# Performance work log

Hardware: AMD Instinct MI355X
Metric: run time of the kernel (lower is better)

Reference implementation:

```python
import jax, jax.numpy as jnp
import numpy as np

L, H, D, FF = 12, 12, 768, 3072          # ViT-B/16
PS, GRID = 16, 14
NP = GRID * GRID                          # 196 patches
NT = NP + 1                               # 197 tokens (cls + patches)
B = 64
NC = 100                                  # classes
POS_G = (0, 1)
POS_E = (2, 3, 4)
LEN_G, LEN_E = 5, 20
GL, EL = len(POS_G), len(POS_E)
E_POOL = 10                               # task_num


def _ln(x, g, b, eps=1e-6):
    m = x.mean(-1, keepdims=True)
    v = ((x - m) ** 2).mean(-1, keepdims=True)
    return (x - m) * jax.lax.rsqrt(v + eps) * g + b


def _mlp(x, w1, b1, w2, b2):
    return jax.nn.gelu(x @ w1.T + b1, approximate=False) @ w2.T + b2


def _attn(q, k, v):
    # q: [B,Nq,C], k/v: [B,Nk,C] (Nk may include prefix prompt tokens)
    Bq, Nq, C = q.shape
    hd = C // H
    q = q.reshape(Bq, Nq, H, hd).transpose(0, 2, 1, 3)
    k = k.reshape(Bq, -1, H, hd).transpose(0, 2, 1, 3)
    v = v.reshape(Bq, -1, H, hd).transpose(0, 2, 1, 3)
    a = jax.nn.softmax(jnp.einsum('bhqd,bhkd->bhqk', q, k) * (hd ** -0.5), axis=-1)
    o = jnp.einsum('bhqk,bhkd->bhqd', a, v)
    return o.transpose(0, 2, 1, 3).reshape(Bq, Nq, C)


def setup_inputs() -> dict:
    key = jax.random.key(0)
    ks = iter(jax.random.split(key, 24))
    s = 0.02
    return {
        'inputs':    jax.random.normal(next(ks), (B, 3, 224, 224), jnp.float32),
        'patch_w':   jax.random.normal(next(ks), (D, 3, PS, PS), jnp.float32) * s,
        'patch_b':   jnp.zeros((D,), jnp.float32),
        'cls_token': jax.random.normal(next(ks), (1, 1, D), jnp.float32) * s,
        'pos_embed': jax.random.normal(next(ks), (1, NT, D), jnp.float32) * s,
        'ln1_g':  jnp.ones((L, D), jnp.float32),
        'ln1_b':  jnp.zeros((L, D), jnp.float32),
        'qkv_w':  jax.random.normal(next(ks), (L, 3 * D, D), jnp.float32) * s,
        'qkv_b':  jnp.zeros((L, 3 * D), jnp.float32),
        'proj_w': jax.random.normal(next(ks), (L, D, D), jnp.float32) * s,
        'proj_b': jnp.zeros((L, D), jnp.float32),
        'ln2_g':  jnp.ones((L, D), jnp.float32),
        'ln2_b':  jnp.zeros((L, D), jnp.float32),
        'fc1_w':  jax.random.normal(next(ks), (L, FF, D), jnp.float32) * s,
        'fc1_b':  jnp.zeros((L, FF), jnp.float32),
        'fc2_w':  jax.random.normal(next(ks), (L, D, FF), jnp.float32) * s,
        'fc2_b':  jnp.zeros((L, D), jnp.float32),
        'norm_g': jnp.ones((D,), jnp.float32),
        'norm_b': jnp.zeros((D,), jnp.float32),
        'head_w': jax.random.normal(next(ks), (NC, D), jnp.float32) * s,
        'head_b': jnp.zeros((NC,), jnp.float32),
        'g_prompt': jax.random.normal(next(ks), (1, 2 * GL * LEN_G, D), jnp.float32) * s,
        'e_key':    jax.random.normal(next(ks), (E_POOL, D), jnp.float32),
        'e_prompt': jax.random.normal(next(ks), (E_POOL, 2 * EL * LEN_E, D), jnp.float32) * s,
    }


def _forward(inputs, patch_w, patch_b, cls_token, pos_embed, ln1_g, ln1_b,
             qkv_w, qkv_b, proj_w, proj_b, ln2_g, ln2_b, fc1_w, fc1_b,
             fc2_w, fc2_b, norm_g, norm_b, head_w, head_b,
             g_prompt, e_key, e_prompt):
    Bn = inputs.shape[0]
    # --- patch embed (conv k16 s16 == unfold + linear); under torch.no_grad ---
    x = inputs.reshape(Bn, 3, GRID, PS, GRID, PS).transpose(0, 2, 4, 1, 3, 5)
    x = x.reshape(Bn, NP, 3 * PS * PS) @ patch_w.reshape(D, -1).T + patch_b
    tok = jnp.concatenate([jnp.broadcast_to(cls_token, (Bn, 1, D)), x], axis=1)
    tok = jax.lax.stop_gradient(tok)  # token_appended computed in no_grad block
    # --- frozen query pass through plain ViT blocks ---
    q = tok + pos_embed
    for i in range(L):
        xn = _ln(q, ln1_g[i], ln1_b[i])
        qq, kk, vv = jnp.split(xn @ qkv_w[i].T + qkv_b[i], 3, axis=-1)
        q = q + _attn(qq, kk, vv) @ proj_w[i].T + proj_b[i]
        q = q + _mlp(_ln(q, ln2_g[i], ln2_b[i]), fc1_w[i], fc1_b[i], fc2_w[i], fc2_b[i])
    query = jax.lax.stop_gradient(_ln(q, norm_g, norm_b)[:, 0])  # [B, D]
    # --- prompt selection (eval path: cosine-sim top-1 from e-pool) ---
    qn = query / jnp.linalg.norm(query, axis=-1, keepdims=True)
    kn = e_key / jnp.linalg.norm(e_key, axis=-1, keepdims=True)
    idx = jnp.argmax(qn @ kn.T, axis=-1)                       # [B]
    cls_pe = pos_embed[0, 0]                                   # [D]
    g_p = jnp.broadcast_to(g_prompt[0].reshape(1, 2 * GL, LEN_G, D),
                           (Bn, 2 * GL, LEN_G, D)) + cls_pe
    e_p = e_prompt[idx].reshape(Bn, 2 * EL, LEN_E, D) + cls_pe
    # --- prefix-tuning pass: prompts concatenated to K/V only ---
    x = tok + pos_embed
    for n in range(L):
        xn = _ln(x, ln1_g[n], ln1_b[n])
        ks_, vs_ = [xn], [xn]
        if n in POS_G:
            j = POS_G.index(n)
            ks_.append(g_p[:, 2 * j]); vs_.append(g_p[:, 2 * j + 1])
        if n in POS_E:
            j = POS_E.index(n)
            ks_.append(e_p[:, 2 * j]); vs_.append(e_p[:, 2 * j + 1])
        xk = jnp.concatenate(ks_, axis=1) if len(ks_) > 1 else xn
        xv = jnp.concatenate(vs_, axis=1) if len(vs_) > 1 else xn
        qh = xn @ qkv_w[n][:D].T + qkv_b[n][:D]
        kh = xk @ qkv_w[n][D:2 * D].T + qkv_b[n][D:2 * D]
        vh = xv @ qkv_w[n][2 * D:].T + qkv_b[n][2 * D:]
        x = x + _attn(qh, kh, vh) @ proj_w[n].T + proj_b[n]
        x = x + _mlp(_ln(x, ln2_g[n], ln2_b[n]), fc1_w[n], fc1_b[n], fc2_w[n], fc2_b[n])
    x = _ln(x, norm_g, norm_b)
    return x[:, 0] @ head_w.T + head_b  # [B, NC]


def reference(inputs, patch_w, patch_b, cls_token, pos_embed, ln1_g, ln1_b,
              qkv_w, qkv_b, proj_w, proj_b, ln2_g, ln2_b, fc1_w, fc1_b,
              fc2_w, fc2_b, norm_g, norm_b, head_w, head_b,
              g_prompt, e_key, e_prompt):
    return _forward(inputs, patch_w, patch_b, cls_token, pos_embed, ln1_g, ln1_b,
                    qkv_w, qkv_b, proj_w, proj_b, ln2_g, ln2_b, fc1_w, fc1_b,
                    fc2_w, fc2_b, norm_g, norm_b, head_w, head_b,
                    g_prompt, e_key, e_prompt)
```

## Files before the change

kernel.cpp:

```cpp
#include <hip/hip_runtime.h>

typedef unsigned short ushort_t;
typedef __attribute__((ext_vector_type(8))) __bf16 bf16x8;
typedef __attribute__((ext_vector_type(4))) float f32x4;
typedef __attribute__((ext_vector_type(4))) unsigned int u32x4;
typedef __attribute__((ext_vector_type(4))) unsigned short u16x4;
typedef __attribute__((ext_vector_type(4))) float fl4;

#define AS1(p) ((const __attribute__((address_space(1))) void*)(p))
#define AS3(p) ((__attribute__((address_space(3))) void*)(p))

__device__ __forceinline__ ushort_t f2bf(float f) {
    unsigned u = __float_as_uint(f);
    u += 0x7FFFu + ((u >> 16) & 1u);
    return (ushort_t)(u >> 16);
}

__device__ __forceinline__ bf16x8 ld_bf8(const ushort_t* p) {
    return __builtin_bit_cast(bf16x8, *(const u32x4*)p);
}

__global__ void cvt_kernel(const float* __restrict__ in, ushort_t* __restrict__ out, int n4)
{
    int i = blockIdx.x * 256 + threadIdx.x;
    if (i >= n4) return;
    fl4 f = ((const fl4*)in)[i];
    u16x4 h;
    h.x = f2bf(f.x); h.y = f2bf(f.y); h.z = f2bf(f.z); h.w = f2bf(f.w);
    ((u16x4*)out)[i] = h;
}

template<int OBF, int ADD, int GELU>
__global__ __launch_bounds__(256)
void gemm_kernel(const ushort_t* __restrict__ A, const ushort_t* __restrict__ W,
                 const float* __restrict__ bias, void* __restrict__ Cv,
                 int M, int N, int K)
{
    __shared__ ushort_t As[128 * 32];
    __shared__ ushort_t Ws[128 * 32];
    const int tid  = threadIdx.x;
    const int lane = tid & 63, wv = tid >> 6;
    const int quad = lane >> 4, l16 = lane & 15;
    const int m0 = blockIdx.x * 128, n0 = blockIdx.y * 128;
    const int wm = (wv >> 1) * 64, wn = (wv & 1) * 64;

    f32x4 acc[4][4];
#pragma unroll
    for (int i = 0; i < 4; ++i)
#pragma unroll
        for (int j = 0; j < 4; ++j) acc[i][j] = (f32x4){0.f, 0.f, 0.f, 0.f};

    const int lr = lane >> 2, lc = (lane & 3) * 8;
    const ushort_t* gA0 = A + (size_t)(m0 + wv * 16 + lr) * K + lc;
    const ushort_t* gA1 = gA0 + (size_t)64 * K;
    const ushort_t* gW0 = W + (size_t)(n0 + wv * 16 + lr) * K + lc;
    const ushort_t* gW1 = gW0 + (size_t)64 * K;
    ushort_t* lA0 = As + wv * 512;
    ushort_t* lA1 = As + (wv + 4) * 512;
    ushort_t* lW0 = Ws + wv * 512;
    ushort_t* lW1 = Ws + (wv + 4) * 512;

    for (int kt = 0; kt < K; kt += 32) {
        __builtin_amdgcn_global_load_lds(AS1(gA0 + kt), AS3(lA0), 16, 0, 0);
        __builtin_amdgcn_global_load_lds(AS1(gA1 + kt), AS3(lA1), 16, 0, 0);
        __builtin_amdgcn_global_load_lds(AS1(gW0 + kt), AS3(lW0), 16, 0, 0);
        __builtin_amdgcn_global_load_lds(AS1(gW1 + kt), AS3(lW1), 16, 0, 0);
        __syncthreads();
        bf16x8 af[4], bfr[4];
#pragma unroll
        for (int i = 0; i < 4; ++i) af[i]  = ld_bf8(As + (wm + i * 16 + l16) * 32 + quad * 8);
#pragma unroll
        for (int j = 0; j < 4; ++j) bfr[j] = ld_bf8(Ws + (wn + j * 16 + l16) * 32 + quad * 8);
#pragma unroll
        for (int i = 0; i < 4; ++i)
#pragma unroll
            for (int j = 0; j < 4; ++j)
                acc[i][j] = __builtin_amdgcn_mfma_f32_16x16x32_bf16(af[i], bfr[j], acc[i][j], 0, 0, 0);
        __syncthreads();
    }

    float* Cf = (float*)Cv;
    ushort_t* Ch = (ushort_t*)Cv;
#pragma unroll
    for (int j = 0; j < 4; ++j) {
        int n = n0 + wn + j * 16 + l16;
        float bv = bias[n];
#pragma unroll
        for (int i = 0; i < 4; ++i) {
            int mb = m0 + wm + i * 16 + quad * 4;
#pragma unroll
            for (int r = 0; r < 4; ++r) {
                int m = mb + r;
                if (m < M) {
                    float v = acc[i][j][r] + bv;
                    if (GELU) v = 0.5f * v * (1.f + erff(v * 0.70710678118654752f));
                    size_t off = (size_t)m * N + n;
                    if (OBF) {
                        Ch[off] = f2bf(v);
                    } else {
                        float o = v;
                        if (ADD) o += Cf[off];
                        Cf[off] = o;
                    }
                }
            }
        }
    }
}

__global__ __launch_bounds__(256)
void attn_kernel(const ushort_t* __restrict__ qkv, const ushort_t* __restrict__ pk,
                 const ushort_t* __restrict__ pv, int plen, int pbs,
                 ushort_t* __restrict__ out)
{
    __shared__ ushort_t KV[224 * 72];
    __shared__ ushort_t Ps[64 * 232];
    const int tid  = threadIdx.x;
    const int lane = tid & 63, wv = tid >> 6;
    const int quad = lane >> 4, l16 = lane & 15;
    const int b = blockIdx.x / 12, h = blockIdx.x % 12;
    const int q0 = blockIdx.y * 64;
    const int Nk = 197 + plen;

    for (int i = tid; i < 224 * 8; i += 256) {
        int tok = i >> 3, c = (i & 7) * 8;
        u32x4 v = (u32x4){0, 0, 0, 0};
        if (tok < 197)
            v = *(const u32x4*)(qkv + (size_t)(b * 197 + tok) * 2304 + 768 + h * 64 + c);
        else if (tok < Nk)
            v = *(const u32x4*)(pk + (size_t)(b * pbs + (tok - 197)) * 768 + h * 64 + c);
        *(u32x4*)(KV + tok * 72 + c) = v;
    }
    __syncthreads();

    bf16x8 qf0 = __builtin_bit_cast(bf16x8, (u32x4){0, 0, 0, 0});
    bf16x8 qf1 = qf0;
    int qrow = q0 + wv * 16 + l16;
    if (qrow < 197) {
        const ushort_t* qp = qkv + (size_t)(b * 197 + qrow) * 2304 + h * 64 + quad * 8;
        qf0 = ld_bf8(qp);
        qf1 = ld_bf8(qp + 32);
    }

    f32x4 sarr[14];
#pragma unroll
    for (int t = 0; t < 14; ++t) {
        f32x4 s = (f32x4){0.f, 0.f, 0.f, 0.f};
        bf16x8 k0 = ld_bf8(KV + (t * 16 + l16) * 72 + quad * 8);
        bf16x8 k1 = ld_bf8(KV + (t * 16 + l16) * 72 + 32 + quad * 8);
        s = __builtin_amdgcn_mfma_f32_16x16x32_bf16(qf0, k0, s, 0, 0, 0);
        s = __builtin_amdgcn_mfma_f32_16x16x32_bf16(qf1, k1, s, 0, 0, 0);
        if (t * 16 + l16 >= Nk) s = (f32x4){-1e30f, -1e30f, -1e30f, -1e30f};
        sarr[t] = s;
    }

    float mx[4] = {-1e30f, -1e30f, -1e30f, -1e30f};
#pragma unroll
    for (int t = 0; t < 14; ++t)
#pragma unroll
        for (int r = 0; r < 4; ++r) mx[r] = fmaxf(mx[r], sarr[t][r]);
#pragma unroll
    for (int off = 8; off >= 1; off >>= 1)
#pragma unroll
        for (int r = 0; r < 4; ++r) mx[r] = fmaxf(mx[r], __shfl_xor(mx[r], off));

    float sm[4] = {0.f, 0.f, 0.f, 0.f};
#pragma unroll
    for (int t = 0; t < 14; ++t)
#pragma unroll
        for (int r = 0; r < 4; ++r) {
            float p = __expf((sarr[t][r] - mx[r]) * 0.125f);
            sm[r] += p;
            Ps[(wv * 16 + quad * 4 + r) * 232 + t * 16 + l16] = f2bf(p);
        }
#pragma unroll
    for (int off = 8; off >= 1; off >>= 1)
#pragma unroll
        for (int r = 0; r < 4; ++r) sm[r] += __shfl_xor(sm[r], off);
    float rs[4];
#pragma unroll
    for (int r = 0; r < 4; ++r) rs[r] = 1.f / sm[r];
    __syncthreads();

    for (int i = tid; i < 224 * 8; i += 256) {
        int tok = i >> 3, c = (i & 7) * 8;
        u32x4 v = (u32x4){0, 0, 0, 0};
        if (tok < 197)
            v = *(const u32x4*)(qkv + (size_t)(b * 197 + tok) * 2304 + 1536 + h * 64 + c);
        else if (tok < Nk)
            v = *(const u32x4*)(pv + (size_t)(b * pbs + (tok - 197)) * 768 + h * 64 + c);
        ushort_t tmp[8];
        *(u32x4*)tmp = v;
#pragma unroll
        for (int jj = 0; jj < 8; ++jj) KV[(c + jj) * 232 + tok] = tmp[jj];
    }
    __syncthreads();

    f32x4 oc[4];
#pragma unroll
    for (int j = 0; j < 4; ++j) oc[j] = (f32x4){0.f, 0.f, 0.f, 0.f};
#pragma unroll
    for (int ks = 0; ks < 7; ++ks) {
        bf16x8 pf = ld_bf8(Ps + (wv * 16 + l16) * 232 + ks * 32 + quad * 8);
#pragma unroll
        for (int j = 0; j < 4; ++j) {
            bf16x8 vf = ld_bf8(KV + (j * 16 + l16) * 232 + ks * 32 + quad * 8);
            oc[j] = __builtin_amdgcn_mfma_f32_16x16x32_bf16(pf, vf, oc[j], 0, 0, 0);
        }
    }
#pragma unroll
    for (int j = 0; j < 4; ++j) {
        int hd = h * 64 + j * 16 + l16;
#pragma unroll
        for (int r = 0; r < 4; ++r) {
            int qr = q0 + wv * 16 + quad * 4 + r;
            if (qr < 197) out[(size_t)(b * 197 + qr) * 768 + hd] = f2bf(oc[j][r] * rs[r]);
        }
    }
}

__global__ __launch_bounds__(256)
void ln_kernel(const float* __restrict__ x, const float* __restrict__ g,
               const float* __restrict__ bt, ushort_t* __restrict__ out)
{
    const int row = blockIdx.x, tid = threadIdx.x;
    const float* xr = x + (size_t)row * 768;
    float v0 = xr[tid], v1 = xr[tid + 256], v2 = xr[tid + 512];
    float s = v0 + v1 + v2;
    float s2 = v0 * v0 + v1 * v1 + v2 * v2;
#pragma unroll
    for (int off = 32; off >= 1; off >>= 1) {
        s  += __shfl_xor(s, off);
        s2 += __shfl_xor(s2, off);
    }
    __shared__ float red[8];
    if ((tid & 63) == 0) { red[tid >> 6] = s; red[(tid >> 6) + 4] = s2; }
    __syncthreads();
    float S  = red[0] + red[1] + red[2] + red[3];
    float S2 = red[4] + red[5] + red[6] + red[7];
    float mean = S * (1.f / 768.f);
    float var  = fmaxf(S2 * (1.f / 768.f) - mean * mean, 0.f);
    float rstd = rsqrtf(var + 1e-6f);
    size_t o = (size_t)row * 768;
    out[o + tid]       = f2bf((v0 - mean) * rstd * g[tid]       + bt[tid]);
    out[o + tid + 256] = f2bf((v1 - mean) * rstd * g[tid + 256] + bt[tid + 256]);
    out[o + tid + 512] = f2bf((v2 - mean) * rstd * g[tid + 512] + bt[tid + 512]);
}

__global__ __launch_bounds__(256)
void ln_cls_kernel(const float* __restrict__ x, const float* __restrict__ g,
                   const float* __restrict__ bt, float* __restrict__ out)
{
    const int b = blockIdx.x, tid = threadIdx.x;
    const float* xr = x + (size_t)b * 197 * 768;
    float v0 = xr[tid], v1 = xr[tid + 256], v2 = xr[tid + 512];
    float s = v0 + v1 + v2;
    float s2 = v0 * v0 + v1 * v1 + v2 * v2;
#pragma unroll
    for (int off = 32; off >= 1; off >>= 1) {
        s  += __shfl_xor(s, off);
        s2 += __shfl_xor(s2, off);
    }
    __shared__ float red[8];
    if ((tid & 63) == 0) { red[tid >> 6] = s; red[(tid >> 6) + 4] = s2; }
    __syncthreads();
    float S  = red[0] + red[1] + red[2] + red[3];
    float S2 = red[4] + red[5] + red[6] + red[7];
    float mean = S * (1.f / 768.f);
    float var  = fmaxf(S2 * (1.f / 768.f) - mean * mean, 0.f);
    float rstd = rsqrtf(var + 1e-6f);
    out[b * 768 + tid]       = (v0 - mean) * rstd * g[tid]       + bt[tid];
    out[b * 768 + tid + 256] = (v1 - mean) * rstd * g[tid + 256] + bt[tid + 256];
    out[b * 768 + tid + 512] = (v2 - mean) * rstd * g[tid + 512] + bt[tid + 512];
}

__device__ __forceinline__ float block_sum(float v, float* red, int tid)
{
#pragma unroll
    for (int off = 32; off >= 1; off >>= 1) v += __shfl_xor(v, off);
    __syncthreads();
    if ((tid & 63) == 0) red[tid >> 6] = v;
    __syncthreads();
    return red[0] + red[1] + red[2] + red[3];
}

__global__ __launch_bounds__(256)
void select_kernel(const float* __restrict__ q, const float* __restrict__ ek,
                   int* __restrict__ idx)
{
    __shared__ float red[4];
    int b = blockIdx.x, tid = threadIdx.x;
    const float* qr = q + b * 768;
    float q0 = qr[tid], q1 = qr[tid + 256], q2 = qr[tid + 512];
    float qq = block_sum(q0 * q0 + q1 * q1 + q2 * q2, red, tid);
    float best = -1e30f; int bi = 0;
    for (int p = 0; p < 10; ++p) {
        const float* kr = ek + p * 768;
        float k0 = kr[tid], k1 = kr[tid + 256], k2 = kr[tid + 512];
        float dt = block_sum(q0 * k0 + q1 * k1 + q2 * k2, red, tid);
        float kk = block_sum(k0 * k0 + k1 * k1 + k2 * k2, red, tid);
        float sim = dt / sqrtf(qq * kk);
        if (sim > best) { best = sim; bi = p; }
    }
    if (tid == 0) idx[b] = bi;
}

__global__ void im2col_kernel(const float* __restrict__ in, ushort_t* __restrict__ out)
{
    int i = blockIdx.x * 256 + threadIdx.x;
    int k = i % 768, m = i / 768;
    int b = m / 196, p = m % 196;
    int gy = p / 14, gx = p % 14;
    int c = k >> 8, r = k & 255, py = r >> 4, px = r & 15;
    out[i] = f2bf(in[(size_t)((b * 3 + c) * 224 + gy * 16 + py) * 224 + gx * 16 + px]);
}

__global__ void assemble_kernel(const float* __restrict__ pt, const float* __restrict__ cls,
                                const float* __restrict__ pos, float* __restrict__ x0)
{
    int i = blockIdx.x * 256 + threadIdx.x;
    int d = i % 768, m = i / 768;
    int bb = m / 197, t = m % 197;
    float v = (t == 0) ? cls[d] : pt[(size_t)(bb * 196 + t - 1) * 768 + d];
    x0[i] = v + pos[t * 768 + d];
}

__global__ void build_gtok_kernel(const float* __restrict__ gp, const float* __restrict__ pos,
                                  ushort_t* __restrict__ out, int sel)
{
    int i = blockIdx.x * 256 + threadIdx.x;
    int d = i % 768, t = i / 768;
    out[i] = f2bf(gp[(sel * 5 + t) * 768 + d] + pos[d]);
}

__global__ void build_etok_kernel(const float* __restrict__ ep, const float* __restrict__ pos,
                                  const int* __restrict__ idx, ushort_t* __restrict__ out, int sel)
{
    int i = blockIdx.x * 256 + threadIdx.x;
    int d = i % 768;
    int t = (i / 768) % 20;
    int b = i / (768 * 20);
    out[i] = f2bf(ep[((size_t)idx[b] * 120 + sel * 20 + t) * 768 + d] + pos[d]);
}

__global__ __launch_bounds__(256)
void head_kernel(const float* __restrict__ cl, const float* __restrict__ hw,
                 const float* __restrict__ hb, float* __restrict__ out)
{
    __shared__ float row[768];
    int b = blockIdx.x, tid = threadIdx.x;
    row[tid]       = cl[b * 768 + tid];
    row[tid + 256] = cl[b * 768 + tid + 256];
    row[tid + 512] = cl[b * 768 + tid + 512];
    __syncthreads();
    for (int c = tid; c < 100; c += 256) {
        float a = hb[c];
        for (int d = 0; d < 768; ++d) a += row[d] * hw[(size_t)c * 768 + d];
        out[b * 100 + c] = a;
    }
}

extern "C" void kernel_launch(void* const* d_in, const int* in_sizes, int n_in,
                              void* d_out, int out_size, void* d_ws, size_t ws_size,
                              hipStream_t stream)
{
    const float* inputs   = (const float*)d_in[0];
    const float* patch_w  = (const float*)d_in[1];
    const float* patch_b  = (const float*)d_in[2];
    const float* cls_tok  = (const float*)d_in[3];
    const float* pos_emb  = (const float*)d_in[4];
    const float* ln1_g    = (const float*)d_in[5];
    const float* ln1_b    = (const float*)d_in[6];
    const float* qkv_w    = (const float*)d_in[7];
    const float* qkv_b    = (const float*)d_in[8];
    const float* proj_w   = (const float*)d_in[9];
    const float* proj_b   = (const float*)d_in[10];
    const float* ln2_g    = (const float*)d_in[11];
    const float* ln2_b    = (const float*)d_in[12];
    const float* fc1_w    = (const float*)d_in[13];
    const float* fc1_b    = (const float*)d_in[14];
    const float* fc2_w    = (const float*)d_in[15];
    const float* fc2_b    = (const float*)d_in[16];
    const float* norm_g   = (const float*)d_in[17];
    const float* norm_b   = (const float*)d_in[18];
    const float* head_w   = (const float*)d_in[19];
    const float* head_b   = (const float*)d_in[20];
    const float* g_prompt = (const float*)d_in[21];
    const float* e_key    = (const float*)d_in[22];
    const float* e_prompt = (const float*)d_in[23];

    char* wp = (char*)d_ws;
    auto carve = [&](size_t bytes) {
        char* p = wp;
        wp += (bytes + 255) & ~(size_t)255;
        return p;
    };
    ushort_t* wqkv = (ushort_t*)carve(12ull * 2304 * 768 * 2);
    ushort_t* wprj = (ushort_t*)carve(12ull * 768 * 768 * 2);
    ushort_t* wfc1 = (ushort_t*)carve(12ull * 3072 * 768 * 2);
    ushort_t* wfc2 = (ushort_t*)carve(12ull * 768 * 3072 * 2);
    ushort_t* wpat = (ushort_t*)carve(768ull * 768 * 2);
    float*    x     = (float*)   carve(12608ull * 768 * 4);
    ushort_t* xn    = (ushort_t*)carve(12672ull * 768 * 2);
    ushort_t* big   = (ushort_t*)carve(12672ull * 3072 * 2);
    ushort_t* ptk   = (ushort_t*)carve(1280ull * 768 * 2);
    ushort_t* pK    = (ushort_t*)carve(1280ull * 768 * 2);
    ushort_t* pV    = (ushort_t*)carve(1280ull * 768 * 2);
    float*    query = (float*)   carve(64ull * 768 * 4);
    float*    clsln = (float*)   carve(64ull * 768 * 4);
    int*      idx   = (int*)     carve(256);
    (void)ws_size; (void)in_sizes; (void)n_in; (void)out_size;

    cvt_kernel<<<20736, 256, 0, stream>>>(qkv_w,   wqkv, 5308416);
    cvt_kernel<<< 6912, 256, 0, stream>>>(proj_w,  wprj, 1769472);
    cvt_kernel<<<27648, 256, 0, stream>>>(fc1_w,   wfc1, 7077888);
    cvt_kernel<<<27648, 256, 0, stream>>>(fc2_w,   wfc2, 7077888);
    cvt_kernel<<<  576, 256, 0, stream>>>(patch_w, wpat, 147456);

    for (int pass = 0; pass < 2; ++pass) {
        im2col_kernel<<<37632, 256, 0, stream>>>(inputs, xn);
        gemm_kernel<0, 0, 0><<<dim3(98, 6), 256, 0, stream>>>(xn, wpat, patch_b,
                                                              (void*)big, 12544, 768, 768);
        assemble_kernel<<<37824, 256, 0, stream>>>((const float*)big, cls_tok, pos_emb, x);

        for (int l = 0; l < 12; ++l) {
            ln_kernel<<<12608, 256, 0, stream>>>(x, ln1_g + l * 768, ln1_b + l * 768, xn);
            gemm_kernel<1, 0, 0><<<dim3(99, 18), 256, 0, stream>>>(
                xn, wqkv + (size_t)l * 2304 * 768, qkv_b + l * 2304, big, 12608, 2304, 768);

            const ushort_t* pkp = nullptr; const ushort_t* pvp = nullptr;
            int plen = 0, pbs = 0;
            if (pass == 1 && l < 5) {
                const ushort_t* Wk = wqkv + (size_t)l * 2304 * 768 + 768ull * 768;
                const ushort_t* Wv = wqkv + (size_t)l * 2304 * 768 + 1536ull * 768;
                const float* bk = qkv_b + l * 2304 + 768;
                const float* bv = qkv_b + l * 2304 + 1536;
                if (l < 2) {
                    build_gtok_kernel<<<15, 256, 0, stream>>>(g_prompt, pos_emb, ptk, 2 * l);
                    gemm_kernel<1, 0, 0><<<dim3(1, 6), 256, 0, stream>>>(ptk, Wk, bk, pK, 5, 768, 768);
                    build_gtok_kernel<<<15, 256, 0, stream>>>(g_prompt, pos_emb, ptk, 2 * l + 1);
                    gemm_kernel<1, 0, 0><<<dim3(1, 6), 256, 0, stream>>>(ptk, Wv, bv, pV, 5, 768, 768);
                    pkp = pK; pvp = pV; plen = 5; pbs = 0;
                } else {
                    int j = l - 2;
                    build_etok_kernel<<<3840, 256, 0, stream>>>(e_prompt, pos_emb, idx, ptk, 2 * j);
                    gemm_kernel<1, 0, 0><<<dim3(10, 6), 256, 0, stream>>>(ptk, Wk, bk, pK, 1280, 768, 768);
                    build_etok_kernel<<<3840, 256, 0, stream>>>(e_prompt, pos_emb, idx, ptk, 2 * j + 1);
                    gemm_kernel<1, 0, 0><<<dim3(10, 6), 256, 0, stream>>>(ptk, Wv, bv, pV, 1280, 768, 768);
                    pkp = pK; pvp = pV; plen = 20; pbs = 20;
                }
            }
            attn_kernel<<<dim3(768, 4), 256, 0, stream>>>(big, pkp, pvp, plen, pbs, xn);
            gemm_kernel<0, 1, 0><<<dim3(99, 6), 256, 0, stream>>>(
                xn, wprj + (size_t)l * 768 * 768, proj_b + l * 768, x, 12608, 768, 768);
            ln_kernel<<<12608, 256, 0, stream>>>(x, ln2_g + l * 768, ln2_b + l * 768, xn);
            gemm_kernel<1, 0, 1><<<dim3(99, 24), 256, 0, stream>>>(
                xn, wfc1 + (size_t)l * 3072 * 768, fc1_b + l * 3072, big, 12608, 3072, 768);
            gemm_kernel<0, 1, 0><<<dim3(99, 6), 256, 0, stream>>>(
                big, wfc2 + (size_t)l * 768 * 3072, fc2_b + l * 768, x, 12608, 768, 3072);
        }
        if (pass == 0) {
            ln_cls_kernel<<<64, 256, 0, stream>>>(x, norm_g, norm_b, query);
            select_kernel<<<64, 256, 0, stream>>>(query, e_key, idx);
        } else {
            ln_cls_kernel<<<64, 256, 0, stream>>>(x, norm_g, norm_b, clsln);
            head_kernel<<<64, 256, 0, stream>>>(clsln, head_w, head_b, (float*)d_out);
        }
    }
}
```

Measured before the change: 13.90 ms.

## Swizzle GEMM tile order, transpose MFMA output for vector stores, use tanh GELU

The GEMM grid becomes 1D and block IDs are remapped into groups of 8 M-tiles that sweep the N-tiles together, which should improve L2 reuse of the A and W tiles. The MFMA operands are swapped so each lane holds four consecutive N columns, letting the epilogue use vectorized bias loads and 4-wide bf16/float stores and read-modify-writes instead of scalar ones. The exact erf GELU is replaced with a tanh-style approximation via exp, which is cheaper but deviates from the reference's exact GELU.

```diff
diff --git a/kernel.cpp b/kernel.cpp
--- a/kernel.cpp
+++ b/kernel.cpp
@@ -20,6 +20,12 @@
     return __builtin_bit_cast(bf16x8, *(const u32x4*)p);
 }
 
+__device__ __forceinline__ float gelu_f(float x) {
+    float z = 1.5957691216057308f * (x + 0.044715f * x * x * x);
+    float e = __expf(z);
+    return x * e / (e + 1.f);
+}
+
 __global__ void cvt_kernel(const float* __restrict__ in, ushort_t* __restrict__ out, int n4)
 {
     int i = blockIdx.x * 256 + threadIdx.x;
@@ -34,21 +40,31 @@
 __global__ __launch_bounds__(256)
 void gemm_kernel(const ushort_t* __restrict__ A, const ushort_t* __restrict__ W,
                  const float* __restrict__ bias, void* __restrict__ Cv,
-                 int M, int N, int K)
+                 int M, int N, int K, int ntiles)
 {
     __shared__ ushort_t As[128 * 32];
     __shared__ ushort_t Ws[128 * 32];
     const int tid  = threadIdx.x;
     const int lane = tid & 63, wv = tid >> 6;
     const int quad = lane >> 4, l16 = lane & 15;
-    const int m0 = blockIdx.x * 128, n0 = blockIdx.y * 128;
+
+    const int mtiles = gridDim.x / ntiles;
+    const int GM = 8;
+    int gsz = GM * ntiles;
+    int grp = blockIdx.x / gsz;
+    int fm  = grp * GM;
+    int gm  = min(GM, mtiles - fm);
+    int ing = blockIdx.x - grp * gsz;
+    const int m0 = (fm + ing % gm) * 128;
+    const int n0 = (ing / gm) * 128;
+
     const int wm = (wv >> 1) * 64, wn = (wv & 1) * 64;
 
     f32x4 acc[4][4];
 #pragma unroll
-    for (int i = 0; i < 4; ++i)
-#pragma unroll
-        for (int j = 0; j < 4; ++j) acc[i][j] = (f32x4){0.f, 0.f, 0.f, 0.f};
+    for (int j = 0; j < 4; ++j)
+#pragma unroll
+        for (int i = 0; i < 4; ++i) acc[j][i] = (f32x4){0.f, 0.f, 0.f, 0.f};
 
     const int lr = lane >> 2, lc = (lane & 3) * 8;
     const ushort_t* gA0 = A + (size_t)(m0 + wv * 16 + lr) * K + lc;
@@ -72,37 +88,46 @@
 #pragma unroll
         for (int j = 0; j < 4; ++j) bfr[j] = ld_bf8(Ws + (wn + j * 16 + l16) * 32 + quad * 8);
 #pragma unroll
-        for (int i = 0; i < 4; ++i)
-#pragma unroll
-            for (int j = 0; j < 4; ++j)
-                acc[i][j] = __builtin_amdgcn_mfma_f32_16x16x32_bf16(af[i], bfr[j], acc[i][j], 0, 0, 0);
+        for (int j = 0; j < 4; ++j)
+#pragma unroll
+            for (int i = 0; i < 4; ++i)
+                acc[j][i] = __builtin_amdgcn_mfma_f32_16x16x32_bf16(bfr[j], af[i], acc[j][i], 0, 0, 0);
         __syncthreads();
     }
 
     float* Cf = (float*)Cv;
     ushort_t* Ch = (ushort_t*)Cv;
-#pragma unroll
-    for (int j = 0; j < 4; ++j) {
-        int n = n0 + wn + j * 16 + l16;
-        float bv = bias[n];
-#pragma unroll
-        for (int i = 0; i < 4; ++i) {
-            int mb = m0 + wm + i * 16 + quad * 4;
+    fl4 bv[4];
+#pragma unroll
+    for (int j = 0; j < 4; ++j) bv[j] = *(const fl4*)(bias + n0 + wn + j * 16 + quad * 4);
+
+#pragma unroll
+    for (int i = 0; i < 4; ++i) {
+        int m = m0 + wm + i * 16 + l16;
+        if (m >= M) continue;
+        size_t rowoff = (size_t)m * N;
+#pragma unroll
+        for (int j = 0; j < 4; ++j) {
+            int nb = n0 + wn + j * 16 + quad * 4;
+            float vals[4];
 #pragma unroll
             for (int r = 0; r < 4; ++r) {
-                int m = mb + r;
-                if (m < M) {
-                    float v = acc[i][j][r] + bv;
-                    if (GELU) v = 0.5f * v * (1.f + erff(v * 0.70710678118654752f));
-                    size_t off = (size_t)m * N + n;
-                    if (OBF) {
-                        Ch[off] = f2bf(v);
-                    } else {
-                        float o = v;
-                        if (ADD) o += Cf[off];
-                        Cf[off] = o;
-                    }
+                float v = acc[j][i][r] + bv[j][r];
+                if (GELU) v = gelu_f(v);
+                vals[r] = v;
+            }
+            if (OBF) {
+                u16x4 h;
+                h.x = f2bf(vals[0]); h.y = f2bf(vals[1]);
+                h.z = f2bf(vals[2]); h.w = f2bf(vals[3]);
+                *(u16x4*)(Ch + rowoff + nb) = h;
+            } else {
+                fl4 o = {vals[0], vals[1], vals[2], vals[3]};
+                if (ADD) {
+                    fl4 c = *(const fl4*)(Cf + rowoff + nb);
+                    o.x += c.x; o.y += c.y; o.z += c.z; o.w += c.w;
                 }
+                *(fl4*)(Cf + rowoff + nb) = o;
             }
         }
     }
@@ -419,14 +444,14 @@
 
     for (int pass = 0; pass < 2; ++pass) {
         im2col_kernel<<<37632, 256, 0, stream>>>(inputs, xn);
-        gemm_kernel<0, 0, 0><<<dim3(98, 6), 256, 0, stream>>>(xn, wpat, patch_b,
-                                                              (void*)big, 12544, 768, 768);
+        gemm_kernel<0, 0, 0><<<98 * 6, 256, 0, stream>>>(xn, wpat, patch_b,
+                                                         (void*)big, 12544, 768, 768, 6);
         assemble_kernel<<<37824, 256, 0, stream>>>((const float*)big, cls_tok, pos_emb, x);
 
         for (int l = 0; l < 12; ++l) {
             ln_kernel<<<12608, 256, 0, stream>>>(x, ln1_g + l * 768, ln1_b + l * 768, xn);
-            gemm_kernel<1, 0, 0><<<dim3(99, 18), 256, 0, stream>>>(
-                xn, wqkv + (size_t)l * 2304 * 768, qkv_b + l * 2304, big, 12608, 2304, 768);
+            gemm_kernel<1, 0, 0><<<99 * 18, 256, 0, stream>>>(
+                xn, wqkv + (size_t)l * 2304 * 768, qkv_b + l * 2304, big, 12608, 2304, 768, 18);
 
             const ushort_t* pkp = nullptr; const ushort_t* pvp = nullptr;
             int plen = 0, pbs = 0;
@@ -437,27 +462,27 @@
                 const float* bv = qkv_b + l * 2304 + 1536;
                 if (l < 2) {
                     build_gtok_kernel<<<15, 256, 0, stream>>>(g_prompt, pos_emb, ptk, 2 * l);
-                    gemm_kernel<1, 0, 0><<<dim3(1, 6), 256, 0, stream>>>(ptk, Wk, bk, pK, 5, 768, 768);
+                    gemm_kernel<1, 0, 0><<<6, 256, 0, stream>>>(ptk, Wk, bk, pK, 5, 768, 768, 6);
                     build_gtok_kernel<<<15, 256, 0, stream>>>(g_prompt, pos_emb, ptk, 2 * l + 1);
-                    gemm_kernel<1, 0, 0><<<dim3(1, 6), 256, 0, stream>>>(ptk, Wv, bv, pV, 5, 768, 768);
+                    gemm_kernel<1, 0, 0><<<6, 256, 0, stream>>>(ptk, Wv, bv, pV, 5, 768, 768, 6);
                     pkp = pK; pvp = pV; plen = 5; pbs = 0;
                 } else {
                     int j = l - 2;
                     build_etok_kernel<<<3840, 256, 0, stream>>>(e_prompt, pos_emb, idx, ptk, 2 * j);
-                    gemm_kernel<1, 0, 0><<<dim3(10, 6), 256, 0, stream>>>(ptk, Wk, bk, pK, 1280, 768, 768);
+                    gemm_kernel<1, 0, 0><<<10 * 6, 256, 0, stream>>>(ptk, Wk, bk, pK, 1280, 768, 768, 6);
                     build_etok_kernel<<<3840, 256, 0, stream>>>(e_prompt, pos_emb, idx, ptk, 2 * j + 1);
-                    gemm_kernel<1, 0, 0><<<dim3(10, 6), 256, 0, stream>>>(ptk, Wv, bv, pV, 1280, 768, 768);
+                    gemm_kernel<1, 0, 0><<<10 * 6, 256, 0, stream>>>(ptk, Wv, bv, pV, 1280, 768, 768, 6);
                     pkp = pK; pvp = pV; plen = 20; pbs = 20;
                 }
             }
             attn_kernel<<<dim3(768, 4), 256, 0, stream>>>(big, pkp, pvp, plen, pbs, xn);
-            gemm_kernel<0, 1, 0><<<dim3(99, 6), 256, 0, stream>>>(
-                xn, wprj + (size_t)l * 768 * 768, proj_b + l * 768, x, 12608, 768, 768);
+            gemm_kernel<0, 1, 0><<<99 * 6, 256, 0, stream>>>(
+                xn, wprj + (size_t)l * 768 * 768, proj_b + l * 768, x, 12608, 768, 768, 6);
             ln_kernel<<<12608, 256, 0, stream>>>(x, ln2_g + l * 768, ln2_b + l * 768, xn);
-            gemm_kernel<1, 0, 1><<<dim3(99, 24), 256, 0, stream>>>(
-                xn, wfc1 + (size_t)l * 3072 * 768, fc1_b + l * 3072, big, 12608, 3072, 768);
-            gemm_kernel<0, 1, 0><<<dim3(99, 6), 256, 0, stream>>>(
-                big, wfc2 + (size_t)l * 768 * 3072, fc2_b + l * 768, x, 12608, 768, 3072);
+            gemm_kernel<1, 0, 1><<<99 * 24, 256, 0, stream>>>(
+                xn, wfc1 + (size_t)l * 3072 * 768, fc1_b + l * 3072, big, 12608, 3072, 768, 24);
+            gemm_kernel<0, 1, 0><<<99 * 6, 256, 0, stream>>>(
+                big, wfc2 + (size_t)l * 768 * 3072, fc2_b + l * 768, x, 12608, 768, 3072, 6);
         }
         if (pass == 0) {
             ln_cls_kernel<<<64, 256, 0, stream>>>(x, norm_g, norm_b, query);
```

After: 12.26 ms. -11.8%, faster.
